# Optimization experiments

Measured on AMD Instinct MI355X. Metric: run time of the kernel, lower is better.

## Reference

```python
import jax, jax.numpy as jnp
import numpy as np

B, S, D = 8, 2048, 1024


def setup_inputs() -> dict:
    key = jax.random.key(0)
    k1, k2, k3, k4 = jax.random.split(key, 4)
    scale = 1.0 / np.sqrt(D)
    x = jax.random.normal(k1, (B, S, D), dtype=jnp.float32)
    Wq = jax.random.normal(k2, (D, D), dtype=jnp.float32) * scale
    Wk = jax.random.normal(k3, (D, D), dtype=jnp.float32) * scale
    Wv = jax.random.normal(k4, (D, D), dtype=jnp.float32) * scale
    return {"x": x, "Wq": Wq, "Wk": Wk, "Wv": Wv}


def reference(x, Wq, Wk, Wv):
    # nn.Linear(d, d, bias=False): y = x @ W.T
    q = jnp.einsum('bsd,ed->bse', x, Wq)
    k = jnp.einsum('bsd,ed->bse', x, Wk)
    v = jnp.einsum('bsd,ed->bse', x, Wv)
    S_len = x.shape[1]
    d_k = k.shape[-1]
    # full score matrix, causal mask (strict upper triangle -> -inf)
    scores = jnp.einsum('bqd,bkd->bqk', q, k)
    causal = jnp.triu(jnp.ones((S_len, S_len), dtype=bool), k=1)
    scores = jnp.where(causal[None, :, :], -jnp.inf, scores)
    attn = jax.nn.softmax(scores / jnp.sqrt(jnp.asarray(d_k, scores.dtype)), axis=-1)
    # dropout p=0.0 (eval) -> identity
    return jnp.einsum('bqk,bkd->bqd', attn, v)
```

## Files before the change

### kernel.cpp

```cpp
#include <hip/hip_runtime.h>


typedef _Float16 v8h __attribute__((ext_vector_type(8)));
typedef _Float16 v4h __attribute__((ext_vector_type(4)));
typedef float    v4f __attribute__((ext_vector_type(4)));

#define BM 256
#define BN 256

__device__ __forceinline__ void async16(const _Float16* g, _Float16* l) {
  __builtin_amdgcn_global_load_lds(
      (__attribute__((address_space(1))) void*)(void*)g,
      (__attribute__((address_space(3))) void*)l, 16, 0, 0);
}

__device__ __forceinline__ void rd_a(const _Float16* U, int offA0, int base,
                                     v8h a[4]) {
#pragma unroll
  for (int i = 0; i < 4; ++i) a[i] = *(const v8h*)(U + offA0 + (base + i) * 512);
}
__device__ __forceinline__ void rd_b(const _Float16* U, int offB0, v8h b[4]) {
#pragma unroll
  for (int j = 0; j < 4; ++j) b[j] = *(const v8h*)(U + offB0 + j * 512);
}

__device__ __forceinline__ void mfma16(const v8h a[4], const v8h b[4],
                                       v4f (*accr)[4]) {
  __builtin_amdgcn_s_setprio(1);
#pragma unroll
  for (int i = 0; i < 4; ++i)
#pragma unroll
    for (int j = 0; j < 4; ++j)
      accr[i][j] = __builtin_amdgcn_mfma_f32_16x16x32_f16(a[i], b[j],
                                                          accr[i][j], 0, 0, 0);
  __builtin_amdgcn_s_setprio(0);
}

#define VM8 asm volatile("s_waitcnt vmcnt(8)" ::: "memory")
#define VM4 asm volatile("s_waitcnt vmcnt(4)" ::: "memory")
#define VM0 asm volatile("s_waitcnt vmcnt(0)" ::: "memory")
#define LG8                                                                  \
  asm volatile("s_waitcnt lgkmcnt(8)" ::: "memory");                         \
  __builtin_amdgcn_sched_barrier(0)
#define LG4                                                                  \
  asm volatile("s_waitcnt lgkmcnt(4)" ::: "memory");                         \
  __builtin_amdgcn_sched_barrier(0)
#define LG0                                                                  \
  asm volatile("s_waitcnt lgkmcnt(0)" ::: "memory");                         \
  __builtin_amdgcn_sched_barrier(0)
#define BAR __builtin_amdgcn_s_barrier()

__device__ __forceinline__ void gemm_loop(const _Float16* Ab, int lda,
                                          const _Float16* Bb, int ldb,
                                          int NKT, _Float16* lds,
                                          int w, int lane, int wr, int wc,
                                          int lr, int quad, v4f acc[8][4]) {
  const int offA0 = (wr + lr) * 32 + ((quad ^ (((wr + lr) >> 1) & 3)) * 8);
  const int offB0 = 8192 + (wc + lr) * 32 + ((quad ^ (((wc + lr) >> 1) & 3)) * 8);

  const int u0 = w * 128 + lane;
  const int u1 = u0 + 64;
  const int r0 = u0 >> 2, c0 = (u0 & 3) ^ ((r0 >> 1) & 3);
  const int r1 = u1 >> 2, c1 = (u1 & 3) ^ ((r1 >> 1) & 3);
  const _Float16* pA0 = Ab + (size_t)r0 * lda + c0 * 8;
  const _Float16* pA1 = Ab + (size_t)r1 * lda + c1 * 8;
  const _Float16* pB0 = Bb + (size_t)r0 * ldb + c0 * 8;
  const _Float16* pB1 = Bb + (size_t)r1 * ldb + c1 * 8;
  const int dA0 = (w * 128) * 8;
  const int dA1 = (w * 128 + 64) * 8;

#define STAGE(T)                                                             \
  do {                                                                       \
    _Float16* Ld = lds + ((T) & 3) * 16384;                                  \
    async16(pA0 + (T) * 32, Ld + dA0);                                       \
    async16(pB0 + (T) * 32, Ld + 8192 + dA0);                                \
    async16(pA1 + (T) * 32, Ld + dA1);                                       \
    async16(pB1 + (T) * 32, Ld + 8192 + dA1);                                \
  } while (0)
#define SL(T) (lds + ((T) & 3) * 16384)

  v8h aLo[4], aHi[4], bE[4], bO[4];

  STAGE(0);
  STAGE(1);
  STAGE(2);
  VM8;
  BAR;
  rd_a(SL(0), offA0, 0, aLo);
  rd_b(SL(0), offB0, bE);

  for (int t2 = 0; t2 < NKT - 4; t2 += 2) {
    VM8; BAR;
    rd_a(SL(t2), offA0, 4, aHi);
    STAGE(t2 + 3);
    LG4; mfma16(aLo, bE, &acc[0]);
    VM8; BAR;
    rd_a(SL(t2 + 1), offA0, 0, aLo);
    rd_b(SL(t2 + 1), offB0, bO);
    LG8; mfma16(aHi, bE, &acc[4]);
    VM8; BAR;
    rd_a(SL(t2 + 1), offA0, 4, aHi);
    STAGE(t2 + 4);
    LG4; mfma16(aLo, bO, &acc[0]);
    VM8; BAR;
    rd_a(SL(t2 + 2), offA0, 0, aLo);
    rd_b(SL(t2 + 2), offB0, bE);
    LG8; mfma16(aHi, bO, &acc[4]);
  }

  VM8; BAR;
  rd_a(SL(NKT - 4), offA0, 4, aHi);
  STAGE(NKT - 1);
  LG4; mfma16(aLo, bE, &acc[0]);
  VM8; BAR;
  rd_a(SL(NKT - 3), offA0, 0, aLo);
  rd_b(SL(NKT - 3), offB0, bO);
  LG8; mfma16(aHi, bE, &acc[4]);
  VM8; BAR;
  rd_a(SL(NKT - 3), offA0, 4, aHi);
  LG4; mfma16(aLo, bO, &acc[0]);
  VM4; BAR;
  rd_a(SL(NKT - 2), offA0, 0, aLo);
  rd_b(SL(NKT - 2), offB0, bE);
  LG8; mfma16(aHi, bO, &acc[4]);

  VM4; BAR;
  rd_a(SL(NKT - 2), offA0, 4, aHi);
  LG4; mfma16(aLo, bE, &acc[0]);
  VM0; BAR;
  rd_a(SL(NKT - 1), offA0, 0, aLo);
  rd_b(SL(NKT - 1), offB0, bO);
  LG8; mfma16(aHi, bE, &acc[4]);
  BAR;
  rd_a(SL(NKT - 1), offA0, 4, aHi);
  LG4; mfma16(aLo, bO, &acc[0]);
  LG0; mfma16(aHi, bO, &acc[4]);
#undef STAGE
#undef SL
}

__device__ __forceinline__ void grid_swz(int& bx, int& by) {
  const int gx = gridDim.x;
  const int n = gx * gridDim.y;
  const int f = blockIdx.x + blockIdx.y * gx;
  const int s = (f & 7) * (n >> 3) + (f >> 3);
  bx = s % gx;
  by = s / gx;
}

__global__ __launch_bounds__(256)
void cvt_f16(const float* __restrict__ src, _Float16* __restrict__ dst) {
  const int i = (blockIdx.x * 256 + threadIdx.x) * 8;
  float4 a = *(const float4*)(src + i);
  float4 b = *(const float4*)(src + i + 4);
  v8h o = {(_Float16)a.x, (_Float16)a.y, (_Float16)a.z, (_Float16)a.w,
           (_Float16)b.x, (_Float16)b.y, (_Float16)b.z, (_Float16)b.w};
  *(v8h*)(dst + i) = o;
}

__global__ __launch_bounds__(512, 2)
void proj_gemm(const _Float16* __restrict__ X, const _Float16* __restrict__ W,
               _Float16* __restrict__ Qb, _Float16* __restrict__ Kb,
               _Float16* __restrict__ Vt) {
  __shared__ _Float16 lds[65536];
  const int tid = threadIdx.x;
  int bx, by;
  grid_swz(bx, by);
  const int n0 = bx * BN, m0 = by * BM;
  const int which = n0 >> 10;
  const int nw = n0 & 1023;

  const int lane = tid & 63, w = tid >> 6;
  const int wr = (w >> 2) * 128, wc = (w & 3) * 64;
  const int lr = lane & 15, quad = lane >> 4;

  v4f acc[8][4];
#pragma unroll
  for (int i = 0; i < 8; ++i)
#pragma unroll
    for (int j = 0; j < 4; ++j) acc[i][j] = (v4f){0.f, 0.f, 0.f, 0.f};

  gemm_loop(X + (size_t)m0 * 1024, 1024, W + (size_t)n0 * 1024, 1024,
            32, lds, w, lane, wr, wc, lr, quad, acc);

#pragma unroll
  for (int i = 0; i < 8; ++i) {
    const int r0 = m0 + wr + i * 16 + quad * 4;
#pragma unroll
    for (int j = 0; j < 4; ++j) {
      const int cl = wc + j * 16 + lr;
      if (which < 2) {
        _Float16* dst = (which == 0) ? Qb : Kb;
        const int col = nw + cl;
#pragma unroll
        for (int rg = 0; rg < 4; ++rg)
          dst[(size_t)(r0 + rg) * 1024 + col] = (_Float16)acc[i][j][rg];
      } else {
        const int d = nw + cl;
        const int b = r0 >> 11, s = r0 & 2047;
        v4h o = {(_Float16)acc[i][j][0], (_Float16)acc[i][j][1],
                 (_Float16)acc[i][j][2], (_Float16)acc[i][j][3]};
        *(v4h*)(Vt + (size_t)b * 1024 * 2048 + (size_t)d * 2048 + s) = o;
      }
    }
  }
}

__global__ __launch_bounds__(512, 2)
void scores_gemm(const _Float16* __restrict__ Q, const _Float16* __restrict__ K,
                 _Float16* __restrict__ Sc) {
  __shared__ _Float16 lds[65536];
  const int tid = threadIdx.x;
  int bx, by;
  grid_swz(bx, by);
  const int bz = blockIdx.z;
  const int n0 = bx * BN, m0 = by * BM;
  _Float16* Cb = Sc + (size_t)bz * 2048 * 2048;

  if (bx > by) return;

  const _Float16* Qz = Q + (size_t)bz * 2048 * 1024;
  const _Float16* Kz = K + (size_t)bz * 2048 * 1024;

  const int lane = tid & 63, w = tid >> 6;
  const int wr = (w >> 2) * 128, wc = (w & 3) * 64;
  const int lr = lane & 15, quad = lane >> 4;

  v4f acc[8][4];
#pragma unroll
  for (int i = 0; i < 8; ++i)
#pragma unroll
    for (int j = 0; j < 4; ++j) acc[i][j] = (v4f){0.f, 0.f, 0.f, 0.f};

  gemm_loop(Qz + (size_t)m0 * 1024, 1024, Kz + (size_t)n0 * 1024, 1024,
            32, lds, w, lane, wr, wc, lr, quad, acc);

  const _Float16 ninf = (_Float16)(-__builtin_inff());
#pragma unroll
  for (int i = 0; i < 8; ++i) {
    const int r0 = m0 + wr + i * 16 + quad * 4;
#pragma unroll
    for (int j = 0; j < 4; ++j) {
      const int cc = n0 + wc + j * 16 + lr;
#pragma unroll
      for (int rg = 0; rg < 4; ++rg) {
        const int rr = r0 + rg;
        Cb[(size_t)rr * 2048 + cc] = (cc > rr) ? ninf : (_Float16)acc[i][j][rg];
      }
    }
  }
}

__global__ __launch_bounds__(256)
void softmax_rows(_Float16* __restrict__ Sc) {
  _Float16* base = Sc + (size_t)blockIdx.x * 2048;
  const int q = blockIdx.x & 2047;
  const int ktile = ((q >> 8) + 1) << 8;
  const int tid = threadIdx.x;
  const int lane = tid & 63, w = tid >> 6;
  const bool active = tid * 8 < ktile;

  float f[8];
  if (active) {
    v8h pv = *(const v8h*)(base + tid * 8);
#pragma unroll
    for (int j = 0; j < 8; ++j) f[j] = (float)pv[j];
  } else {
#pragma unroll
    for (int j = 0; j < 8; ++j) f[j] = -__builtin_inff();
  }

  float mx = f[0];
#pragma unroll
  for (int j = 1; j < 8; ++j) mx = fmaxf(mx, f[j]);
#pragma unroll
  for (int off = 32; off; off >>= 1) mx = fmaxf(mx, __shfl_xor(mx, off));
  __shared__ float redm[4], reds[4];
  if (lane == 0) redm[w] = mx;
  __syncthreads();
  mx = fmaxf(fmaxf(redm[0], redm[1]), fmaxf(redm[2], redm[3]));

  const float scale = 0.03125f;
  float e[8], s = 0.f;
#pragma unroll
  for (int j = 0; j < 8; ++j) {
    e[j] = __expf((f[j] - mx) * scale);
    s += e[j];
  }
#pragma unroll
  for (int off = 32; off; off >>= 1) s += __shfl_xor(s, off);
  if (lane == 0) reds[w] = s;
  __syncthreads();
  s = reds[0] + reds[1] + reds[2] + reds[3];
  const float inv = 1.0f / s;
  if (active) {
    v8h pv;
#pragma unroll
    for (int j = 0; j < 8; ++j) pv[j] = (_Float16)(e[j] * inv);
    *(v8h*)(base + tid * 8) = pv;
  }
}

__global__ __launch_bounds__(512, 2)
void pv_gemm(const _Float16* __restrict__ P, const _Float16* __restrict__ Vt,
             float* __restrict__ Out) {
  __shared__ _Float16 lds[65536];
  const int tid = threadIdx.x;
  int bx, by;
  grid_swz(bx, by);
  const int bz = blockIdx.z;
  const int n0 = bx * BN, m0 = by * BM;
  const _Float16* Pb = P + (size_t)bz * 2048 * 2048;
  const _Float16* Vb = Vt + (size_t)bz * 1024 * 2048;
  float* Cb = Out + (size_t)bz * 2048 * 1024;

  const int lane = tid & 63, w = tid >> 6;
  const int wr = (w >> 2) * 128, wc = (w & 3) * 64;
  const int lr = lane & 15, quad = lane >> 4;

  v4f acc[8][4];
#pragma unroll
  for (int i = 0; i < 8; ++i)
#pragma unroll
    for (int j = 0; j < 4; ++j) acc[i][j] = (v4f){0.f, 0.f, 0.f, 0.f};

  gemm_loop(Pb + (size_t)m0 * 2048, 2048, Vb + (size_t)n0 * 2048, 2048,
            (by + 1) * 8, lds, w, lane, wr, wc, lr, quad, acc);

#pragma unroll
  for (int i = 0; i < 8; ++i) {
    const int r0 = m0 + wr + i * 16 + quad * 4;
#pragma unroll
    for (int j = 0; j < 4; ++j) {
      const int cc = n0 + wc + j * 16 + lr;
#pragma unroll
      for (int rg = 0; rg < 4; ++rg)
        Cb[(size_t)(r0 + rg) * 1024 + cc] = acc[i][j][rg];
    }
  }
}

extern "C" void kernel_launch(void* const* d_in, const int* in_sizes, int n_in,
                              void* d_out, int out_size, void* d_ws, size_t ws_size,
                              hipStream_t stream) {
  const int B = 8, S = 2048, D = 1024;
  const int M = B * S;
  const float* x  = (const float*)d_in[0];
  const float* Wq = (const float*)d_in[1];
  const float* Wk = (const float*)d_in[2];
  const float* Wv = (const float*)d_in[3];
  float* out = (float*)d_out;

  char* ws = (char*)d_ws;
  _Float16* Qb = (_Float16*)ws;
  _Float16* Kb = (_Float16*)(ws + (size_t)33554432);
  _Float16* Vt = (_Float16*)(ws + (size_t)67108864);
  _Float16* Sc = (_Float16*)(ws + (size_t)100663296);
  _Float16* xh = Sc;
  _Float16* Wh = Sc + (size_t)M * D;

  cvt_f16<<<(M * D) / 2048, 256, 0, stream>>>(x, xh);
  cvt_f16<<<(D * D) / 2048, 256, 0, stream>>>(Wq, Wh);
  cvt_f16<<<(D * D) / 2048, 256, 0, stream>>>(Wk, Wh + (size_t)D * D);
  cvt_f16<<<(D * D) / 2048, 256, 0, stream>>>(Wv, Wh + (size_t)2 * D * D);

  proj_gemm<<<dim3(12, M / BM, 1), 512, 0, stream>>>(xh, Wh, Qb, Kb, Vt);

  scores_gemm<<<dim3(S / BN, S / BM, B), 512, 0, stream>>>(Qb, Kb, Sc);

  softmax_rows<<<B * S, 256, 0, stream>>>(Sc);

  pv_gemm<<<dim3(D / BN, S / BM, B), 512, 0, stream>>>(Sc, Vt, out);
}
```

Before: 397.1 us.

## Use 128x128 tiles with triangular scheduling for causal scores and PV GEMMs

Scores GEMM moves from 256x256 tiles to 128x128 tiles with a linear triangular launch, so no blocks are spent on masked tiles and the masked region is finer-grained. The PV GEMM pairs row tiles i and 15-i in one block so each block does the same K work, and it also uses 128-tile causal truncation. Softmax row extent is tightened to 128 granularity, and the three weight conversions are merged into one launch. The cost is a simpler, less software-pipelined GEMM loop with a barrier every K step, and less data reuse per tile.

```diff
diff --git a/kernel.cpp b/kernel.cpp
--- a/kernel.cpp
+++ b/kernel.cpp
@@ -49,6 +49,7 @@
   asm volatile("s_waitcnt lgkmcnt(0)" ::: "memory");                         \
   __builtin_amdgcn_sched_barrier(0)
 #define BAR __builtin_amdgcn_s_barrier()
+#define SBAR __builtin_amdgcn_sched_barrier(0)
 
 __device__ __forceinline__ void gemm_loop(const _Float16* Ab, int lda,
                                           const _Float16* Bb, int ldb,
@@ -139,6 +140,55 @@
 #undef SL
 }
 
+__device__ __forceinline__ void gemm128(const _Float16* Ab, int lda,
+                                        const _Float16* Bb, int ldb,
+                                        int NKT, _Float16* lds,
+                                        int w, int lane, int wr, int wc,
+                                        int lr, int quad, v4f acc[4][4]) {
+  const int offA0 = (wr + lr) * 32 + ((quad ^ (((wr + lr) >> 1) & 3)) * 8);
+  const int offB0 = 4096 + (wc + lr) * 32 + ((quad ^ (((wc + lr) >> 1) & 3)) * 8);
+
+  const int u0 = w * 128 + lane;
+  const int u1 = u0 + 64;
+  const int r0 = u0 >> 2, c0 = (u0 & 3) ^ ((r0 >> 1) & 3);
+  const int r1 = u1 >> 2, c1 = (u1 & 3) ^ ((r1 >> 1) & 3);
+  const _Float16* pA0 = Ab + (size_t)r0 * lda + c0 * 8;
+  const _Float16* pA1 = Ab + (size_t)r1 * lda + c1 * 8;
+  const _Float16* pB0 = Bb + (size_t)r0 * ldb + c0 * 8;
+  const _Float16* pB1 = Bb + (size_t)r1 * ldb + c1 * 8;
+  const int dA0 = (w * 128) * 8;
+  const int dA1 = (w * 128 + 64) * 8;
+
+#define STAGE(T)                                                             \
+  do {                                                                       \
+    _Float16* Ld = lds + ((T) & 3) * 8192;                                   \
+    async16(pA0 + (T) * 32, Ld + dA0);                                       \
+    async16(pA1 + (T) * 32, Ld + dA1);                                       \
+    async16(pB0 + (T) * 32, Ld + 4096 + dA0);                                \
+    async16(pB1 + (T) * 32, Ld + 4096 + dA1);                                \
+  } while (0)
+
+  STAGE(0);
+  STAGE(1);
+  STAGE(2);
+  VM8;
+  BAR;
+
+  for (int t = 0; t < NKT; ++t) {
+    const _Float16* U = lds + (t & 3) * 8192;
+    v8h a[4], b[4];
+    rd_a(U, offA0, 0, a);
+    rd_b(U, offB0, b);
+    if (t < NKT - 2) { VM4; } else { VM0; }
+    BAR;
+    SBAR;
+    if (t + 3 < NKT) STAGE(t + 3);
+    LG0;
+    mfma16(a, b, &acc[0]);
+  }
+#undef STAGE
+}
+
 __device__ __forceinline__ void grid_swz(int& bx, int& by) {
   const int gx = gridDim.x;
   const int n = gx * gridDim.y;
@@ -156,6 +206,20 @@
   v8h o = {(_Float16)a.x, (_Float16)a.y, (_Float16)a.z, (_Float16)a.w,
            (_Float16)b.x, (_Float16)b.y, (_Float16)b.z, (_Float16)b.w};
   *(v8h*)(dst + i) = o;
+}
+
+__global__ __launch_bounds__(256)
+void cvt_f16_w(const float* __restrict__ Wq, const float* __restrict__ Wk,
+               const float* __restrict__ Wv, _Float16* __restrict__ dst) {
+  const int bid = blockIdx.x;
+  const int m = bid >> 9;
+  const float* src = (m == 0) ? Wq : (m == 1) ? Wk : Wv;
+  const int i = ((bid & 511) * 256 + threadIdx.x) * 8;
+  float4 a = *(const float4*)(src + i);
+  float4 b = *(const float4*)(src + i + 4);
+  v8h o = {(_Float16)a.x, (_Float16)a.y, (_Float16)a.z, (_Float16)a.w,
+           (_Float16)b.x, (_Float16)b.y, (_Float16)b.z, (_Float16)b.w};
+  *(v8h*)(dst + (size_t)m * 1048576 + i) = o;
 }
 
 __global__ __launch_bounds__(512, 2)
@@ -206,38 +270,40 @@
   }
 }
 
-__global__ __launch_bounds__(512, 2)
+__global__ __launch_bounds__(256, 2)
 void scores_gemm(const _Float16* __restrict__ Q, const _Float16* __restrict__ K,
                  _Float16* __restrict__ Sc) {
-  __shared__ _Float16 lds[65536];
+  __shared__ _Float16 lds[32768];
   const int tid = threadIdx.x;
-  int bx, by;
-  grid_swz(bx, by);
-  const int bz = blockIdx.z;
-  const int n0 = bx * BN, m0 = by * BM;
+  const int t1d = blockIdx.x;
+  const int bz = blockIdx.y;
+
+  int by = 0;
+  while ((by + 1) * (by + 2) / 2 <= t1d) ++by;
+  const int bx = t1d - by * (by + 1) / 2;
+
+  const int m0 = by * 128, n0 = bx * 128;
   _Float16* Cb = Sc + (size_t)bz * 2048 * 2048;
-
-  if (bx > by) return;
-
   const _Float16* Qz = Q + (size_t)bz * 2048 * 1024;
   const _Float16* Kz = K + (size_t)bz * 2048 * 1024;
 
   const int lane = tid & 63, w = tid >> 6;
-  const int wr = (w >> 2) * 128, wc = (w & 3) * 64;
+  const int wr = (w >> 1) * 64, wc = (w & 1) * 64;
   const int lr = lane & 15, quad = lane >> 4;
 
-  v4f acc[8][4];
-#pragma unroll
-  for (int i = 0; i < 8; ++i)
+  v4f acc[4][4];
+#pragma unroll
+  for (int i = 0; i < 4; ++i)
 #pragma unroll
     for (int j = 0; j < 4; ++j) acc[i][j] = (v4f){0.f, 0.f, 0.f, 0.f};
 
-  gemm_loop(Qz + (size_t)m0 * 1024, 1024, Kz + (size_t)n0 * 1024, 1024,
-            32, lds, w, lane, wr, wc, lr, quad, acc);
+  gemm128(Qz + (size_t)m0 * 1024, 1024, Kz + (size_t)n0 * 1024, 1024,
+          32, lds, w, lane, wr, wc, lr, quad, acc);
 
   const _Float16 ninf = (_Float16)(-__builtin_inff());
-#pragma unroll
-  for (int i = 0; i < 8; ++i) {
+  const bool diag = (bx == by);
+#pragma unroll
+  for (int i = 0; i < 4; ++i) {
     const int r0 = m0 + wr + i * 16 + quad * 4;
 #pragma unroll
     for (int j = 0; j < 4; ++j) {
@@ -245,7 +311,8 @@
 #pragma unroll
       for (int rg = 0; rg < 4; ++rg) {
         const int rr = r0 + rg;
-        Cb[(size_t)rr * 2048 + cc] = (cc > rr) ? ninf : (_Float16)acc[i][j][rg];
+        _Float16 v = (_Float16)acc[i][j][rg];
+        Cb[(size_t)rr * 2048 + cc] = (diag && cc > rr) ? ninf : v;
       }
     }
   }
@@ -255,7 +322,7 @@
 void softmax_rows(_Float16* __restrict__ Sc) {
   _Float16* base = Sc + (size_t)blockIdx.x * 2048;
   const int q = blockIdx.x & 2047;
-  const int ktile = ((q >> 8) + 1) << 8;
+  const int ktile = ((q >> 7) + 1) << 7;
   const int tid = threadIdx.x;
   const int lane = tid & 63, w = tid >> 6;
   const bool active = tid * 8 < ktile;
@@ -301,42 +368,50 @@
   }
 }
 
-__global__ __launch_bounds__(512, 2)
+__global__ __launch_bounds__(256, 2)
 void pv_gemm(const _Float16* __restrict__ P, const _Float16* __restrict__ Vt,
              float* __restrict__ Out) {
-  __shared__ _Float16 lds[65536];
+  __shared__ _Float16 lds[32768];
   const int tid = threadIdx.x;
-  int bx, by;
-  grid_swz(bx, by);
+  const int bxx = blockIdx.x;
+  const int pair = blockIdx.y;
   const int bz = blockIdx.z;
-  const int n0 = bx * BN, m0 = by * BM;
+  const int n0 = bxx * 128;
   const _Float16* Pb = P + (size_t)bz * 2048 * 2048;
   const _Float16* Vb = Vt + (size_t)bz * 1024 * 2048;
   float* Cb = Out + (size_t)bz * 2048 * 1024;
 
   const int lane = tid & 63, w = tid >> 6;
-  const int wr = (w >> 2) * 128, wc = (w & 3) * 64;
+  const int wr = (w >> 1) * 64, wc = (w & 1) * 64;
   const int lr = lane & 15, quad = lane >> 4;
 
-  v4f acc[8][4];
-#pragma unroll
-  for (int i = 0; i < 8; ++i)
-#pragma unroll
-    for (int j = 0; j < 4; ++j) acc[i][j] = (v4f){0.f, 0.f, 0.f, 0.f};
-
-  gemm_loop(Pb + (size_t)m0 * 2048, 2048, Vb + (size_t)n0 * 2048, 2048,
-            (by + 1) * 8, lds, w, lane, wr, wc, lr, quad, acc);
-
-#pragma unroll
-  for (int i = 0; i < 8; ++i) {
-    const int r0 = m0 + wr + i * 16 + quad * 4;
-#pragma unroll
-    for (int j = 0; j < 4; ++j) {
-      const int cc = n0 + wc + j * 16 + lr;
-#pragma unroll
-      for (int rg = 0; rg < 4; ++rg)
-        Cb[(size_t)(r0 + rg) * 1024 + cc] = acc[i][j][rg];
+#pragma unroll
+  for (int part = 0; part < 2; ++part) {
+    const int by = part ? (15 - pair) : pair;
+    const int NKT = part ? ((16 - pair) * 4) : ((pair + 1) * 4);
+    const int m0 = by * 128;
+
+    v4f acc[4][4];
+#pragma unroll
+    for (int i = 0; i < 4; ++i)
+#pragma unroll
+      for (int j = 0; j < 4; ++j) acc[i][j] = (v4f){0.f, 0.f, 0.f, 0.f};
+
+    gemm128(Pb + (size_t)m0 * 2048, 2048, Vb + (size_t)n0 * 2048, 2048,
+            NKT, lds, w, lane, wr, wc, lr, quad, acc);
+
+#pragma unroll
+    for (int i = 0; i < 4; ++i) {
+      const int r0 = m0 + wr + i * 16 + quad * 4;
+#pragma unroll
+      for (int j = 0; j < 4; ++j) {
+        const int cc = n0 + wc + j * 16 + lr;
+#pragma unroll
+        for (int rg = 0; rg < 4; ++rg)
+          Cb[(size_t)(r0 + rg) * 1024 + cc] = acc[i][j][rg];
+      }
     }
+    __syncthreads();
   }
 }
 
@@ -360,15 +435,13 @@
   _Float16* Wh = Sc + (size_t)M * D;
 
   cvt_f16<<<(M * D) / 2048, 256, 0, stream>>>(x, xh);
-  cvt_f16<<<(D * D) / 2048, 256, 0, stream>>>(Wq, Wh);
-  cvt_f16<<<(D * D) / 2048, 256, 0, stream>>>(Wk, Wh + (size_t)D * D);
-  cvt_f16<<<(D * D) / 2048, 256, 0, stream>>>(Wv, Wh + (size_t)2 * D * D);
+  cvt_f16_w<<<1536, 256, 0, stream>>>(Wq, Wk, Wv, Wh);
 
   proj_gemm<<<dim3(12, M / BM, 1), 512, 0, stream>>>(xh, Wh, Qb, Kb, Vt);
 
-  scores_gemm<<<dim3(S / BN, S / BM, B), 512, 0, stream>>>(Qb, Kb, Sc);
+  scores_gemm<<<dim3(136, B, 1), 256, 0, stream>>>(Qb, Kb, Sc);
 
   softmax_rows<<<B * S, 256, 0, stream>>>(Sc);
 
-  pv_gemm<<<dim3(D / BN, S / BM, B), 512, 0, stream>>>(Sc, Vt, out);
-}
+  pv_gemm<<<dim3(8, 8, B), 256, 0, stream>>>(Sc, Vt, out);
+}
```

After: 385.9 us. 2.8% less time.
